# Performance work log

Measured on AMD Instinct MI355X. Metric: run time of the kernel, lower is better.

The kernel has to match this reference:

```python
import jax, jax.numpy as jnp
import numpy as np
import math

FLAT_DIM = 30_000_000
SIZE = 1 << 25  # 33_554_432, next pow2 >= FLAT_DIM


def fwht(x):
    """Iterative fast Walsh-Hadamard transform, same butterfly ordering as the torch code."""
    size = x.shape[0]
    h = 1
    while h < size:
        x = x.reshape(-1, 2 * h)
        left, right = x[:, :h], x[:, h:]
        x = jnp.concatenate([left + right, left - right], axis=1)
        h *= 2
    return x.reshape(size)


def setup_inputs() -> dict:
    key = jax.random.key(0)
    k1, k2, k3, k4 = jax.random.split(key, 4)
    theta = jax.random.normal(k1, (FLAT_DIM,), dtype=jnp.float32)
    G = jax.random.normal(k2, (SIZE,), dtype=jnp.float32)
    B = (jax.random.randint(k3, (SIZE,), 0, 2) * 2 - 1).astype(jnp.float32)
    Pi = jax.random.permutation(k4, SIZE)
    divisor = jnp.sqrt(SIZE * jnp.sum(G * G))  # scalar, computed from G as in __init__
    return {"theta": theta, "G": G, "B": B, "divisor": divisor, "Pi": Pi}


def reference(theta, G, B, divisor, Pi):
    flat_dim = theta.shape[0]
    size = G.shape[0]
    theta_padded = jnp.pad(theta, (0, size - flat_dim)) * B
    hbx = fwht(theta_padded)
    pihbx = hbx[Pi]
    gpihbx = pihbx * G
    hgpihbx = fwht(gpihbx)
    result = hgpihbx[:flat_dim]
    scale = divisor * jnp.sqrt(jnp.float32(flat_dim) / jnp.float32(size))
    return result / scale
```

## Files before the change

kernel.cpp:

```cpp
#include <hip/hip_runtime.h>
#include <math.h>

#define SIZE_N   (1 << 25)
#define FLATD    30000000
#define FLATD4   7500000
#define LOW_N    8192

__global__ __launch_bounds__(512) void k1_padB_fwht_low(const float* __restrict__ theta,
                                                        const float* __restrict__ B,
                                                        float* __restrict__ x) {
    __shared__ float lds[LOW_N];
    float4* lds4 = (float4*)lds;
    const int t   = threadIdx.x;
    const int blk = blockIdx.x;
    const int base4 = blk * (LOW_N / 4);
    const float4* B4  = (const float4*)B;
    const float4* th4 = (const float4*)theta;

#pragma unroll
    for (int i = 0; i < 4; ++i) {
        int l4 = t + (i << 9);
        int g4 = base4 + l4;
        float4 b = B4[g4];
        float4 v = make_float4(0.f, 0.f, 0.f, 0.f);
        if (g4 < FLATD4) v = th4[g4];
        v.x *= b.x; v.y *= b.y; v.z *= b.z; v.w *= b.w;
        lds4[l4] = v;
    }

    for (int s = 0; s < 13; ++s) {
        __syncthreads();
        int h = 1 << s;
#pragma unroll
        for (int i = 0; i < 8; ++i) {
            int p   = t + (i << 9);
            int idx = ((p >> s) << (s + 1)) | (p & (h - 1));
            float a = lds[idx];
            float b2 = lds[idx + h];
            lds[idx]     = a + b2;
            lds[idx + h] = a - b2;
        }
    }
    __syncthreads();

    float4* x4 = (float4*)x;
#pragma unroll
    for (int i = 0; i < 4; ++i) {
        int l4 = t + (i << 9);
        x4[base4 + l4] = lds4[l4];
    }
}

__global__ __launch_bounds__(512) void k_high6(float* __restrict__ x, int A4, int R4) {
    __shared__ float lds[64 * 256];
    float4* lds4 = (float4*)lds;
    const int t   = threadIdx.x;
    const int blk = blockIdx.x;
    const int base4 = (blk >> 5) * A4 + (blk & 31) * 64;
    float4* x4 = (float4*)x;

#pragma unroll
    for (int i = 0; i < 8; ++i) {
        int idx = t + (i << 9);
        int row = idx >> 6;
        int l4  = idx & 63;
        lds4[idx] = x4[base4 + row * R4 + l4];
    }

    for (int s = 0; s < 6; ++s) {
        __syncthreads();
        int h = 1 << s;
#pragma unroll
        for (int i = 0; i < 4; ++i) {
            int w  = t + (i << 9);
            int p  = w >> 6;
            int l4 = w & 63;
            int r0 = ((p >> s) << (s + 1)) | (p & (h - 1));
            int a0 = (r0 << 6) | l4;
            int a1 = ((r0 + h) << 6) | l4;
            float4 a = lds4[a0];
            float4 b = lds4[a1];
            lds4[a0] = make_float4(a.x + b.x, a.y + b.y, a.z + b.z, a.w + b.w);
            lds4[a1] = make_float4(a.x - b.x, a.y - b.y, a.z - b.z, a.w - b.w);
        }
    }
    __syncthreads();

#pragma unroll
    for (int i = 0; i < 8; ++i) {
        int idx = t + (i << 9);
        int row = idx >> 6;
        int l4  = idx & 63;
        x4[base4 + row * R4 + l4] = lds4[idx];
    }
}

__global__ __launch_bounds__(512) void k_high6_out(const float* __restrict__ y,
                                                   const float* __restrict__ divisor,
                                                   float* __restrict__ out) {
    __shared__ float lds[64 * 256];
    float4* lds4 = (float4*)lds;
    const int t   = threadIdx.x;
    const int blk = blockIdx.x;
    const int base4 = (blk >> 5) * 2048 + (blk & 31) * 64;
    const float4* y4 = (const float4*)y;

#pragma unroll
    for (int i = 0; i < 8; ++i) {
        int idx = t + (i << 9);
        int row = idx >> 6;
        int l4  = idx & 63;
        lds4[idx] = y4[base4 + row * 131072 + l4];
    }

    const float scale = divisor[0] * sqrtf((float)FLATD / (float)SIZE_N);
    const float inv   = 1.0f / scale;

    for (int s = 0; s < 6; ++s) {
        __syncthreads();
        int h = 1 << s;
#pragma unroll
        for (int i = 0; i < 4; ++i) {
            int w  = t + (i << 9);
            int p  = w >> 6;
            int l4 = w & 63;
            int r0 = ((p >> s) << (s + 1)) | (p & (h - 1));
            int a0 = (r0 << 6) | l4;
            int a1 = ((r0 + h) << 6) | l4;
            float4 a = lds4[a0];
            float4 b = lds4[a1];
            lds4[a0] = make_float4(a.x + b.x, a.y + b.y, a.z + b.z, a.w + b.w);
            lds4[a1] = make_float4(a.x - b.x, a.y - b.y, a.z - b.z, a.w - b.w);
        }
    }
    __syncthreads();

    float4* out4 = (float4*)out;
#pragma unroll
    for (int i = 0; i < 8; ++i) {
        int idx = t + (i << 9);
        int row = idx >> 6;
        int l4  = idx & 63;
        int o4  = base4 + row * 131072 + l4;
        if (o4 < FLATD4) {
            float4 v = lds4[idx];
            v.x *= inv; v.y *= inv; v.z *= inv; v.w *= inv;
            out4[o4] = v;
        }
    }
}

__global__ __launch_bounds__(512) void k3_gather_fwht_low(const float* __restrict__ x,
                                                          const int* __restrict__ Pi,
                                                          const float* __restrict__ G,
                                                          float* __restrict__ y) {
    __shared__ float lds[LOW_N];
    float4* lds4 = (float4*)lds;
    const int t   = threadIdx.x;
    const int blk = blockIdx.x;
    const int base4 = blk * (LOW_N / 4);
    const int4*   Pi4 = (const int4*)Pi;
    const float4* G4  = (const float4*)G;

#pragma unroll
    for (int i = 0; i < 4; ++i) {
        int l4 = t + (i << 9);
        int g4 = base4 + l4;
        int4   p4 = Pi4[g4];
        float4 g  = G4[g4];
        float4 v;
        v.x = x[p4.x] * g.x;
        v.y = x[p4.y] * g.y;
        v.z = x[p4.z] * g.z;
        v.w = x[p4.w] * g.w;
        lds4[l4] = v;
    }

    for (int s = 0; s < 13; ++s) {
        __syncthreads();
        int h = 1 << s;
#pragma unroll
        for (int i = 0; i < 8; ++i) {
            int p   = t + (i << 9);
            int idx = ((p >> s) << (s + 1)) | (p & (h - 1));
            float a = lds[idx];
            float b2 = lds[idx + h];
            lds[idx]     = a + b2;
            lds[idx + h] = a - b2;
        }
    }
    __syncthreads();

    float4* y4 = (float4*)y;
#pragma unroll
    for (int i = 0; i < 4; ++i) {
        int l4 = t + (i << 9);
        y4[base4 + l4] = lds4[l4];
    }
}

extern "C" void kernel_launch(void* const* d_in, const int* in_sizes, int n_in,
                              void* d_out, int out_size, void* d_ws, size_t ws_size,
                              hipStream_t stream) {
    const float* theta   = (const float*)d_in[0];
    const float* G       = (const float*)d_in[1];
    const float* B       = (const float*)d_in[2];
    const float* divisor = (const float*)d_in[3];
    const int*   Pi      = (const int*)d_in[4];
    float* out = (float*)d_out;

    float* x = (float*)d_ws;
    float* y = x + SIZE_N;

    k1_padB_fwht_low<<<SIZE_N / LOW_N, 512, 0, stream>>>(theta, B, x);
    k_high6<<<2048, 512, 0, stream>>>(x, 131072, 2048);
    k_high6<<<2048, 512, 0, stream>>>(x, 2048, 131072);
    k3_gather_fwht_low<<<SIZE_N / LOW_N, 512, 0, stream>>>(x, Pi, G, y);
    k_high6<<<2048, 512, 0, stream>>>(y, 131072, 2048);
    k_high6_out<<<2048, 512, 0, stream>>>(y, divisor, out);
}
```

Measured before the change: 1.306 ms.

## Store intermediate FWHT data transposed so high-stride passes read contiguously

```diff
diff --git a/kernel.cpp b/kernel.cpp
--- a/kernel.cpp
+++ b/kernel.cpp
@@ -6,67 +6,8 @@
 #define FLATD4   7500000
 #define LOW_N    8192
 
-__global__ __launch_bounds__(512) void k1_padB_fwht_low(const float* __restrict__ theta,
-                                                        const float* __restrict__ B,
-                                                        float* __restrict__ x) {
-    __shared__ float lds[LOW_N];
-    float4* lds4 = (float4*)lds;
-    const int t   = threadIdx.x;
-    const int blk = blockIdx.x;
-    const int base4 = blk * (LOW_N / 4);
-    const float4* B4  = (const float4*)B;
-    const float4* th4 = (const float4*)theta;
-
-#pragma unroll
-    for (int i = 0; i < 4; ++i) {
-        int l4 = t + (i << 9);
-        int g4 = base4 + l4;
-        float4 b = B4[g4];
-        float4 v = make_float4(0.f, 0.f, 0.f, 0.f);
-        if (g4 < FLATD4) v = th4[g4];
-        v.x *= b.x; v.y *= b.y; v.z *= b.z; v.w *= b.w;
-        lds4[l4] = v;
-    }
-
-    for (int s = 0; s < 13; ++s) {
-        __syncthreads();
-        int h = 1 << s;
-#pragma unroll
-        for (int i = 0; i < 8; ++i) {
-            int p   = t + (i << 9);
-            int idx = ((p >> s) << (s + 1)) | (p & (h - 1));
-            float a = lds[idx];
-            float b2 = lds[idx + h];
-            lds[idx]     = a + b2;
-            lds[idx + h] = a - b2;
-        }
-    }
-    __syncthreads();
-
-    float4* x4 = (float4*)x;
-#pragma unroll
-    for (int i = 0; i < 4; ++i) {
-        int l4 = t + (i << 9);
-        x4[base4 + l4] = lds4[l4];
-    }
-}
-
-__global__ __launch_bounds__(512) void k_high6(float* __restrict__ x, int A4, int R4) {
-    __shared__ float lds[64 * 256];
-    float4* lds4 = (float4*)lds;
-    const int t   = threadIdx.x;
-    const int blk = blockIdx.x;
-    const int base4 = (blk >> 5) * A4 + (blk & 31) * 64;
-    float4* x4 = (float4*)x;
-
-#pragma unroll
-    for (int i = 0; i < 8; ++i) {
-        int idx = t + (i << 9);
-        int row = idx >> 6;
-        int l4  = idx & 63;
-        lds4[idx] = x4[base4 + row * R4 + l4];
-    }
-
+
+__device__ __forceinline__ void fwht6_rows(float4* lds4, int t) {
     for (int s = 0; s < 6; ++s) {
         __syncthreads();
         int h = 1 << s;
@@ -85,63 +26,136 @@
         }
     }
     __syncthreads();
-
-#pragma unroll
-    for (int i = 0; i < 8; ++i) {
-        int idx = t + (i << 9);
-        int row = idx >> 6;
-        int l4  = idx & 63;
-        x4[base4 + row * R4 + l4] = lds4[idx];
-    }
-}
-
-__global__ __launch_bounds__(512) void k_high6_out(const float* __restrict__ y,
-                                                   const float* __restrict__ divisor,
-                                                   float* __restrict__ out) {
+}
+
+__global__ __launch_bounds__(512) void k1_padB_fwht_low(const float* __restrict__ theta,
+                                                        const float* __restrict__ B,
+                                                        float* __restrict__ z) {
+    __shared__ float lds[LOW_N];
+    float4* lds4 = (float4*)lds;
+    const int t   = threadIdx.x;
+    const int blk = blockIdx.x;
+    const int base4 = blk * 2048;
+    const float4* B4  = (const float4*)B;
+    const float4* th4 = (const float4*)theta;
+
+#pragma unroll
+    for (int i = 0; i < 4; ++i) {
+        int l4 = t + (i << 9);
+        int g4 = base4 + l4;
+        float4 b = B4[g4];
+        float4 v = make_float4(0.f, 0.f, 0.f, 0.f);
+        if (g4 < FLATD4) v = th4[g4];
+        v.x *= b.x; v.y *= b.y; v.z *= b.z; v.w *= b.w;
+        lds4[l4] = v;
+    }
+
+    for (int s = 0; s < 13; ++s) {
+        __syncthreads();
+        int h = 1 << s;
+#pragma unroll
+        for (int i = 0; i < 8; ++i) {
+            int p   = t + (i << 9);
+            int idx = ((p >> s) << (s + 1)) | (p & (h - 1));
+            float a = lds[idx];
+            float b2 = lds[idx + h];
+            lds[idx]     = a + b2;
+            lds[idx + h] = a - b2;
+        }
+    }
+    __syncthreads();
+
+    float4* z4 = (float4*)z;
+    const int top = blk >> 6, mid = blk & 63;
+    const int wbase = top * 131072 + mid * 64;
+#pragma unroll
+    for (int i = 0; i < 4; ++i) {
+        int l4  = t + (i << 9);
+        int lc  = l4 >> 6, li4 = l4 & 63;
+        z4[wbase + lc * 4096 + li4] = lds4[l4];
+    }
+}
+
+__global__ __launch_bounds__(512) void p_mid(const float4* __restrict__ in4,
+                                             float4* __restrict__ out4) {
     __shared__ float lds[64 * 256];
     float4* lds4 = (float4*)lds;
     const int t   = threadIdx.x;
     const int blk = blockIdx.x;
-    const int base4 = (blk >> 5) * 2048 + (blk & 31) * 64;
-    const float4* y4 = (const float4*)y;
-
-#pragma unroll
-    for (int i = 0; i < 8; ++i) {
-        int idx = t + (i << 9);
-        int row = idx >> 6;
-        int l4  = idx & 63;
-        lds4[idx] = y4[base4 + row * 131072 + l4];
+    const int top = blk >> 5, lc = blk & 31;
+    const int rbase = (top * 32 + lc) * 4096;
+
+#pragma unroll
+    for (int i = 0; i < 8; ++i) {
+        int idx = t + (i << 9);
+        lds4[idx] = in4[rbase + idx];
+    }
+
+    fwht6_rows(lds4, t);
+
+    const int wb = lc * 4096 + top * 64;
+#pragma unroll
+    for (int i = 0; i < 8; ++i) {
+        int idx = t + (i << 9);
+        int mid = idx >> 6, li4 = idx & 63;
+        out4[mid * 131072 + wb + li4] = lds4[idx];
+    }
+}
+
+__global__ __launch_bounds__(512) void p_top(const float4* __restrict__ in4,
+                                             float4* __restrict__ out4) {
+    __shared__ float lds[64 * 256];
+    float4* lds4 = (float4*)lds;
+    const int t   = threadIdx.x;
+    const int blk = blockIdx.x;
+    const int mid = blk >> 5, lc = blk & 31;
+    const int rbase = (mid * 32 + lc) * 4096;
+
+#pragma unroll
+    for (int i = 0; i < 8; ++i) {
+        int idx = t + (i << 9);
+        lds4[idx] = in4[rbase + idx];
+    }
+
+    fwht6_rows(lds4, t);
+
+    const int wb = mid * 2048 + lc * 64;
+#pragma unroll
+    for (int i = 0; i < 8; ++i) {
+        int idx = t + (i << 9);
+        int top = idx >> 6, li4 = idx & 63;
+        out4[top * 131072 + wb + li4] = lds4[idx];
+    }
+}
+
+__global__ __launch_bounds__(512) void p_top_out(const float4* __restrict__ in4,
+                                                 const float* __restrict__ divisor,
+                                                 float* __restrict__ out) {
+    __shared__ float lds[64 * 256];
+    float4* lds4 = (float4*)lds;
+    const int t   = threadIdx.x;
+    const int blk = blockIdx.x;
+    const int mid = blk >> 5, lc = blk & 31;
+    const int rbase = (mid * 32 + lc) * 4096;
+
+#pragma unroll
+    for (int i = 0; i < 8; ++i) {
+        int idx = t + (i << 9);
+        lds4[idx] = in4[rbase + idx];
     }
 
     const float scale = divisor[0] * sqrtf((float)FLATD / (float)SIZE_N);
     const float inv   = 1.0f / scale;
 
-    for (int s = 0; s < 6; ++s) {
-        __syncthreads();
-        int h = 1 << s;
-#pragma unroll
-        for (int i = 0; i < 4; ++i) {
-            int w  = t + (i << 9);
-            int p  = w >> 6;
-            int l4 = w & 63;
-            int r0 = ((p >> s) << (s + 1)) | (p & (h - 1));
-            int a0 = (r0 << 6) | l4;
-            int a1 = ((r0 + h) << 6) | l4;
-            float4 a = lds4[a0];
-            float4 b = lds4[a1];
-            lds4[a0] = make_float4(a.x + b.x, a.y + b.y, a.z + b.z, a.w + b.w);
-            lds4[a1] = make_float4(a.x - b.x, a.y - b.y, a.z - b.z, a.w - b.w);
-        }
-    }
-    __syncthreads();
+    fwht6_rows(lds4, t);
 
     float4* out4 = (float4*)out;
-#pragma unroll
-    for (int i = 0; i < 8; ++i) {
-        int idx = t + (i << 9);
-        int row = idx >> 6;
-        int l4  = idx & 63;
-        int o4  = base4 + row * 131072 + l4;
+    const int wb = mid * 2048 + lc * 64;
+#pragma unroll
+    for (int i = 0; i < 8; ++i) {
+        int idx = t + (i << 9);
+        int top = idx >> 6, li4 = idx & 63;
+        int o4  = top * 131072 + wb + li4;
         if (o4 < FLATD4) {
             float4 v = lds4[idx];
             v.x *= inv; v.y *= inv; v.z *= inv; v.w *= inv;
@@ -158,7 +172,7 @@
     float4* lds4 = (float4*)lds;
     const int t   = threadIdx.x;
     const int blk = blockIdx.x;
-    const int base4 = blk * (LOW_N / 4);
+    const int base4 = blk * 2048;
     const int4*   Pi4 = (const int4*)Pi;
     const float4* G4  = (const float4*)G;
 
@@ -192,10 +206,13 @@
     __syncthreads();
 
     float4* y4 = (float4*)y;
-#pragma unroll
-    for (int i = 0; i < 4; ++i) {
-        int l4 = t + (i << 9);
-        y4[base4 + l4] = lds4[l4];
+    const int top = blk >> 6, mid = blk & 63;
+    const int wbase = top * 131072 + mid * 64;
+#pragma unroll
+    for (int i = 0; i < 4; ++i) {
+        int l4  = t + (i << 9);
+        int lc  = l4 >> 6, li4 = l4 & 63;
+        y4[wbase + lc * 4096 + li4] = lds4[l4];
     }
 }
 
@@ -209,13 +226,15 @@
     const int*   Pi      = (const int*)d_in[4];
     float* out = (float*)d_out;
 
-    float* x = (float*)d_ws;
-    float* y = x + SIZE_N;
-
-    k1_padB_fwht_low<<<SIZE_N / LOW_N, 512, 0, stream>>>(theta, B, x);
-    k_high6<<<2048, 512, 0, stream>>>(x, 131072, 2048);
-    k_high6<<<2048, 512, 0, stream>>>(x, 2048, 131072);
-    k3_gather_fwht_low<<<SIZE_N / LOW_N, 512, 0, stream>>>(x, Pi, G, y);
-    k_high6<<<2048, 512, 0, stream>>>(y, 131072, 2048);
-    k_high6_out<<<2048, 512, 0, stream>>>(y, divisor, out);
-}
+    float* bufA = (float*)d_ws;
+    float* bufB = bufA + SIZE_N;
+    float4* A4 = (float4*)bufA;
+    float4* B4w = (float4*)bufB;
+
+    k1_padB_fwht_low<<<4096, 512, 0, stream>>>(theta, B, bufA);
+    p_mid<<<2048, 512, 0, stream>>>(A4, B4w);
+    p_top<<<2048, 512, 0, stream>>>(B4w, A4);
+    k3_gather_fwht_low<<<4096, 512, 0, stream>>>(bufA, Pi, G, bufB);
+    p_mid<<<2048, 512, 0, stream>>>(B4w, A4);
+    p_top_out<<<2048, 512, 0, stream>>>(A4, divisor, out);
+}
```

New measurement: 1.270 ms. 2.7% less time.
